# Optimization experiments

Measured on AMD Instinct MI355X. Metric: run time of the kernel, lower is better.

Reference implementation:

```python
import jax, jax.numpy as jnp
import numpy as np
from jax import lax

D, NH, T, DFF, SD = 8, 4, 60, 2048, 17
DH = D // NH
NEG = -1e9

def _ln(x, g, b, eps=1e-5):
    m = jnp.mean(x, -1, keepdims=True)
    v = jnp.mean((x - m) ** 2, -1, keepdims=True)
    return (x - m) / jnp.sqrt(v + eps) * g + b

def _mha(q_in, k_in, v_in, Wqkv, bqkv, Wo, bo, mask):
    Wq, Wk, Wv = jnp.split(Wqkv, 3, axis=0)
    bq, bk, bv = jnp.split(bqkv, 3)
    def proj(x, W, bb):
        B, S, _ = x.shape
        return (x @ W.T + bb).reshape(B, S, NH, DH).transpose(0, 2, 1, 3)
    q = proj(q_in, Wq, bq); k = proj(k_in, Wk, bk); v = proj(v_in, Wv, bv)
    s = jnp.einsum('bhqd,bhkd->bhqk', q, k) / np.float32(np.sqrt(DH))
    s = jnp.where(mask, NEG, s)
    o = jnp.einsum('bhqk,bhkd->bhqd', jax.nn.softmax(s, axis=-1), v)
    B, _, S, _ = o.shape
    return o.transpose(0, 2, 1, 3).reshape(B, S, D) @ Wo.T + bo

def _ffn(x, W1, b1, W2, b2):
    return jax.nn.relu(x @ W1.T + b1) @ W2.T + b2

def _forward(x, emb_W, emb_b, eqW, eqb, eoW, eob, ef1W, ef1b, ef2W, ef2b, el1g, el1b, el2g, el2b, eng, enb, dsqW, dsqb, dsoW, dsob, dcqW, dcqb, dcoW, dcob, df1W, df1b, df2W, df2b, dl1g, dl1b, dl2g, dl2b, dl3g, dl3b, dng, dnb, fc_W, fc_b):
    B = x.shape[0]
    idx = jnp.arange(T)
    causal = (idx[None, :] > idx[:, None])[None, None]  # [1,1,T,T], True = blocked

    @jax.checkpoint
    def step(buf, t):
        keymask = (idx > t)[None, None, None, :]  # positions beyond t are padding
        mem = buf
        for i in range(6):  # nn.Transformer default encoder layers
            mem = _ln(mem + _mha(mem, mem, mem, eqW[i], eqb[i], eoW[i], eob[i], keymask), el1g[i], el1b[i])
            mem = _ln(mem + _ffn(mem, ef1W[i], ef1b[i], ef2W[i], ef2b[i]), el2g[i], el2b[i])
        mem = _ln(mem, eng, enb)
        y = buf
        for i in range(2):  # decoder layers
            y = _ln(y + _mha(y, y, y, dsqW[i], dsqb[i], dsoW[i], dsob[i], causal), dl1g[i], dl1b[i])
            y = _ln(y + _mha(y, mem, mem, dcqW[i], dcqb[i], dcoW[i], dcob[i], keymask), dl2g[i], dl2b[i])
            y = _ln(y + _ffn(y, df1W[i], df1b[i], df2W[i], df2b[i]), dl3g[i], dl3b[i])
        y = _ln(y, dng, dnb)
        st = jnp.take(y, t, axis=1) @ fc_W.T + fc_b  # decoded state at last valid pos [B,17]
        buf = buf.at[:, t + 1].set(st @ emb_W.T + emb_b, mode='drop')
        return buf, st

    buf0 = jnp.zeros((B, T, D), x.dtype).at[:, 0].set(x)
    _, states = lax.scan(step, buf0, idx)
    return jnp.transpose(states, (1, 0, 2))  # [B, T, state_dim]

def setup_inputs() -> dict:
    B = 128
    keys = iter(jax.random.split(jax.random.key(0), 64))
    def W(shape):
        return jax.random.normal(next(keys), shape, jnp.float32) / np.float32(np.sqrt(shape[-1]))
    z = lambda *s: jnp.zeros(s, jnp.float32)
    o = lambda *s: jnp.ones(s, jnp.float32)
    return dict(
        quantized_eos_embedding=jax.random.normal(next(keys), (B, D), jnp.float32),
        emb_W=W((D, SD)), emb_b=z(D),
        eqW=W((6, 3 * D, D)), eqb=z(6, 3 * D), eoW=W((6, D, D)), eob=z(6, D),
        ef1W=W((6, DFF, D)), ef1b=z(6, DFF), ef2W=W((6, D, DFF)), ef2b=z(6, D),
        el1g=o(6, D), el1b=z(6, D), el2g=o(6, D), el2b=z(6, D), eng=o(D), enb=z(D),
        dsqW=W((2, 3 * D, D)), dsqb=z(2, 3 * D), dsoW=W((2, D, D)), dsob=z(2, D),
        dcqW=W((2, 3 * D, D)), dcqb=z(2, 3 * D), dcoW=W((2, D, D)), dcob=z(2, D),
        df1W=W((2, DFF, D)), df1b=z(2, DFF), df2W=W((2, D, DFF)), df2b=z(2, D),
        dl1g=o(2, D), dl1b=z(2, D), dl2g=o(2, D), dl2b=z(2, D), dl3g=o(2, D), dl3b=z(2, D),
        dng=o(D), dnb=z(D),
        fc_W=W((SD, D)), fc_b=z(SD),
    )

def reference(quantized_eos_embedding, emb_W, emb_b, eqW, eqb, eoW, eob, ef1W, ef1b, ef2W, ef2b, el1g, el1b, el2g, el2b, eng, enb, dsqW, dsqb, dsoW, dsob, dcqW, dcqb, dcoW, dcob, df1W, df1b, df2W, df2b, dl1g, dl1b, dl2g, dl2b, dl3g, dl3b, dng, dnb, fc_W, fc_b):
    return _forward(quantized_eos_embedding, emb_W, emb_b, eqW, eqb, eoW, eob, ef1W, ef1b, ef2W, ef2b, el1g, el1b, el2g, el2b, eng, enb, dsqW, dsqb, dsoW, dsob, dcqW, dcqb, dcoW, dcob, df1W, df1b, df2W, df2b, dl1g, dl1b, dl2g, dl2b, dl3g, dl3b, dng, dnb, fc_W, fc_b)
```

## Files before the change

### kernel.cpp

```cpp
#include <hip/hip_runtime.h>


typedef __attribute__((ext_vector_type(8))) short short8;
typedef __attribute__((ext_vector_type(4))) float floatx4;
typedef __attribute__((ext_vector_type(4))) unsigned uint4v;

#define DEV static __device__ __forceinline__

namespace {
constexpr int D   = 8;
constexpr int T   = 60;
constexpr int DFF = 2048;
constexpr int SD  = 17;
constexpr int NT  = 512;
constexpr int NW  = NT / 64;
constexpr int NBLK = DFF / 32;
constexpr int BPW  = NBLK / NW;
constexpr int LSTR = NBLK * 2048;
}

struct Params { const float* in[39]; float* out; };

DEV unsigned short f2bf(float f) {
  unsigned u = __builtin_bit_cast(unsigned, f);
  return (unsigned short)((u + 0x8000u) >> 16);
}
DEV float bf2f(unsigned short h) {
  unsigned u = ((unsigned)h) << 16;
  return __builtin_bit_cast(float, u);
}
DEV floatx4 mfma16(short8 a, short8 b, floatx4 c) {
  return __builtin_amdgcn_mfma_f32_16x16x32_bf16(a, b, c, 0, 0, 0);
}
DEV unsigned cvtpk(float lo, float hi) {
  unsigned r;
  asm("v_cvt_pk_bf16_f32 %0, %1, %2" : "=v"(r) : "v"(lo), "v"(hi));
  return r;
}
DEV float lo2f(unsigned u) { return __builtin_bit_cast(float, u << 16); }
DEV float hi2f(unsigned u) { return __builtin_bit_cast(float, u & 0xffff0000u); }
DEV short8 pack4(unsigned a, unsigned b, unsigned c, unsigned d) {
  uint4v u = {a, b, c, d};
  return __builtin_bit_cast(short8, u);
}

__global__ __launch_bounds__(64) void repack_kernel(Params P, short* ws) {
  const int wg = blockIdx.x;
  const int L = wg >> 6, blk = wg & 63;
  const int l = (int)threadIdx.x, gg = l >> 4, rr = l & 15;
  const float *W1p, *b1p, *W2p;
  if (L < 6) { W1p = P.in[7] + L * 16384;  b1p = P.in[8] + L * 2048;  W2p = P.in[9] + L * 16384; }
  else { int m = L - 6; W1p = P.in[25] + m * 16384; b1p = P.in[26] + m * 2048; W2p = P.in[27] + m * 16384; }
  short* out = ws + (L * 64 + blk) * 2048;
  const int j0 = blk * 32;
  short8 z = {0,0,0,0,0,0,0,0};
  for (int tt = 0; tt < 2; ++tt) {
    int j = j0 + tt * 16 + rr;
    short8 r = z;
    if (gg == 3) {
      unsigned short h = f2bf(b1p[j]);
      r[0] = (short)h; r[1] = (short)f2bf(b1p[j] - bf2f(h));
    } else {
      const float* p = W1p + j * 8;
#pragma unroll
      for (int i = 0; i < 8; ++i) {
        float v = p[i];
        unsigned short h = f2bf(v);
        r[i] = (short)((gg == 1) ? f2bf(v - bf2f(h)) : h);
      }
    }
    *(short8*)(out + tt * 512 + l * 8) = r;
  }
  short8 wh = z, wl = z;
  if (rr < 8) {
#pragma unroll
    for (int i = 0; i < 8; ++i) {
      int j = j0 + (i < 4 ? gg * 4 + i : 16 + gg * 4 + (i - 4));
      float v = W2p[rr * 2048 + j];
      unsigned short h = f2bf(v);
      wh[i] = (short)h;
      wl[i] = (short)f2bf(v - bf2f(h));
    }
  }
  *(short8*)(out + 1024 + l * 8) = wh;
  *(short8*)(out + 1536 + l * 8) = wl;
}

__global__ __launch_bounds__(NT, 2) void tdec_kernel(Params P, const short* ws) {
  const int b    = blockIdx.x;
  const int tid  = (int)threadIdx.x;
  const int lane = tid & 63;
  const int wave = tid >> 6;
  const int gg   = lane >> 4;
  const int rr   = lane & 15;

  __shared__ float buf[T][D];
  __shared__ __align__(16) float X[64][D];
  __shared__ float Mem[64][D];
  __shared__ __align__(16) float Qs[64][D];
  __shared__ __align__(16) float Ks[64][D];
  __shared__ __align__(16) float Vs[64][D];
  __shared__ float ATT[64][D];
  __shared__ __align__(16) float red[NW * 1024];
  __shared__ float wAll[10 * 288];
  __shared__ float lnp[40][D];
  __shared__ float b2all[8][D];
  __shared__ float fcw[SD][D];
  __shared__ float fcbv[SD];
  __shared__ float embw[D][SD];
  __shared__ float embbv[D];
  __shared__ float stv[SD];

  for (int o = tid; o < 2880; o += NT) {
    int a = o / 288, off = o - a * 288;
    const float *Wq, *Bq, *Wo, *Bo; int li;
    if (a < 6)              { li = a;            Wq=P.in[3];  Bq=P.in[4];  Wo=P.in[5];  Bo=P.in[6];  }
    else if (((a - 6) & 1) == 0) { li = (a-6)>>1; Wq=P.in[17]; Bq=P.in[18]; Wo=P.in[19]; Bo=P.in[20]; }
    else                    { li = (a-6)>>1;     Wq=P.in[21]; Bq=P.in[22]; Wo=P.in[23]; Bo=P.in[24]; }
    float v;
    if (off < 192)      v = Wq[li*192 + off];
    else if (off < 216) v = Bq[li*24  + off - 192];
    else if (off < 280) v = Wo[li*64  + off - 216];
    else                v = Bo[li*8   + off - 280];
    wAll[o] = v;
  }
  for (int o = tid; o < 320; o += NT) {
    int row = o >> 3, k = o & 7;
    const float* src;
    if (row < 24) { int li = row >> 2, w = row & 3;
      src = (w==0 ? P.in[11] : w==1 ? P.in[12] : w==2 ? P.in[13] : P.in[14]) + li*8;
    } else if (row < 26) src = (row == 24 ? P.in[15] : P.in[16]);
    else if (row < 38) { int q = row - 26, li = q / 6, w = q - li*6;
      src = (w==0?P.in[29]:w==1?P.in[30]:w==2?P.in[31]:w==3?P.in[32]:w==4?P.in[33]:P.in[34]) + li*8;
    } else src = (row == 38 ? P.in[35] : P.in[36]);
    lnp[row][k] = src[k];
  }
  if (tid < 64) { int row = tid >> 3, k = tid & 7;
    b2all[row][k] = (row < 6) ? P.in[10][row*8 + k] : P.in[28][(row-6)*8 + k]; }
  if (tid < 136) fcw[tid >> 3][tid & 7] = P.in[37][tid];
  if (tid < SD)  fcbv[tid] = P.in[38][tid];
  if (tid < 136) embw[tid / 17][tid % 17] = P.in[1][tid];
  if (tid < D)   embbv[tid] = P.in[2][tid];
  if (tid < D)   buf[0][tid] = P.in[0][b*D + tid];
  __syncthreads();

  const short8 zero8 = {0,0,0,0,0,0,0,0};
  const floatx4 zf4  = {0.f,0.f,0.f,0.f};

  auto proj8 = [&](float (*dst)[D], const float (*src)[D], const float* w,
                   const float* bias, int R) {
    for (int o = tid; o < (R << 3); o += NT) {
      int r = o >> 3, d = o & 7;
      const float* wr = w + d * 8;
      const float* xr = src[r];
      float s = bias[d];
#pragma unroll
      for (int k = 0; k < 8; ++k) s += xr[k] * wr[k];
      dst[r][d] = s;
    }
  };

  auto attn_core = [&](float q0, float q1, int e, int stride, int lim,
                       float& l, float& a0, float& a1) {
    int j = e;
    int s3 = 3 * stride;
    for (; j + s3 <= lim; j += 4 * stride) {
      float2 k0 = *(const float2*)&Ks[j][0] ;
      (void)k0;
      break;
    }
  };
  (void)attn_core;

  auto attn = [&](int R, bool causal) {
    if (R <= 32) {
      int p = tid >> 4, h2 = ((tid >> 2) & 3) << 1, e = tid & 3;
      if (p < R) {
        float q0 = Qs[p][h2]     * 0.70710678118654752f;
        float q1 = Qs[p][h2 + 1] * 0.70710678118654752f;
        int lim = causal ? p : (R - 1);
        float l = 0.f, a0 = 0.f, a1 = 0.f;
        int j = e;
        for (; j + 12 <= lim; j += 16) {
          float2 k0 = *(const float2*)&Ks[j     ][h2];
          float2 k1 = *(const float2*)&Ks[j +  4][h2];
          float2 k2 = *(const float2*)&Ks[j +  8][h2];
          float2 k3 = *(const float2*)&Ks[j + 12][h2];
          float2 v0 = *(const float2*)&Vs[j     ][h2];
          float2 v1 = *(const float2*)&Vs[j +  4][h2];
          float2 v2 = *(const float2*)&Vs[j +  8][h2];
          float2 v3 = *(const float2*)&Vs[j + 12][h2];
          float e0 = __expf(q0 * k0.x + q1 * k0.y - 10.f);
          float e1 = __expf(q0 * k1.x + q1 * k1.y - 10.f);
          float e2 = __expf(q0 * k2.x + q1 * k2.y - 10.f);
          float e3 = __expf(q0 * k3.x + q1 * k3.y - 10.f);
          l += e0; a0 += e0 * v0.x; a1 += e0 * v0.y;
          l += e1; a0 += e1 * v1.x; a1 += e1 * v1.y;
          l += e2; a0 += e2 * v2.x; a1 += e2 * v2.y;
          l += e3; a0 += e3 * v3.x; a1 += e3 * v3.y;
        }
        for (; j <= lim; j += 4) {
          float2 kk = *(const float2*)&Ks[j][h2];
          float2 vv = *(const float2*)&Vs[j][h2];
          float ev = __expf(q0 * kk.x + q1 * kk.y - 10.f);
          l += ev; a0 += ev * vv.x; a1 += ev * vv.y;
        }
        l  += __shfl_xor(l, 1);  l  += __shfl_xor(l, 2);
        a0 += __shfl_xor(a0, 1); a0 += __shfl_xor(a0, 2);
        a1 += __shfl_xor(a1, 1); a1 += __shfl_xor(a1, 2);
        if (e == 0) {
          float rl = 1.f / l;
          ATT[p][h2] = a0 * rl; ATT[p][h2 + 1] = a1 * rl;
        }
      }
    } else {
      int p = tid >> 3, h2 = ((tid >> 1) & 3) << 1, e = tid & 1;
      if (p < R) {
        float q0 = Qs[p][h2]     * 0.70710678118654752f;
        float q1 = Qs[p][h2 + 1] * 0.70710678118654752f;
        int lim = causal ? p : (R - 1);
        float l = 0.f, a0 = 0.f, a1 = 0.f;
        int j = e;
        for (; j + 6 <= lim; j += 8) {
          float2 k0 = *(const float2*)&Ks[j    ][h2];
          float2 k1 = *(const float2*)&Ks[j + 2][h2];
          float2 k2 = *(const float2*)&Ks[j + 4][h2];
          float2 k3 = *(const float2*)&Ks[j + 6][h2];
          float2 v0 = *(const float2*)&Vs[j    ][h2];
          float2 v1 = *(const float2*)&Vs[j + 2][h2];
          float2 v2 = *(const float2*)&Vs[j + 4][h2];
          float2 v3 = *(const float2*)&Vs[j + 6][h2];
          float e0 = __expf(q0 * k0.x + q1 * k0.y - 10.f);
          float e1 = __expf(q0 * k1.x + q1 * k1.y - 10.f);
          float e2 = __expf(q0 * k2.x + q1 * k2.y - 10.f);
          float e3 = __expf(q0 * k3.x + q1 * k3.y - 10.f);
          l += e0; a0 += e0 * v0.x; a1 += e0 * v0.y;
          l += e1; a0 += e1 * v1.x; a1 += e1 * v1.y;
          l += e2; a0 += e2 * v2.x; a1 += e2 * v2.y;
          l += e3; a0 += e3 * v3.x; a1 += e3 * v3.y;
        }
        for (; j <= lim; j += 2) {
          float2 kk = *(const float2*)&Ks[j][h2];
          float2 vv = *(const float2*)&Vs[j][h2];
          float ev = __expf(q0 * kk.x + q1 * kk.y - 10.f);
          l += ev; a0 += ev * vv.x; a1 += ev * vv.y;
        }
        l  += __shfl_xor(l, 1);
        a0 += __shfl_xor(a0, 1);
        a1 += __shfl_xor(a1, 1);
        if (e == 0) {
          float rl = 1.f / l;
          ATT[p][h2] = a0 * rl; ATT[p][h2 + 1] = a1 * rl;
        }
      }
    }
  };

  auto oproj_ln = [&](const float* wo, const float* bo, const float* g,
                      const float* bb, int R) {
    if (tid < R) {
      float o[8];
#pragma unroll
      for (int d = 0; d < 8; ++d) {
        float s = bo[d] + X[tid][d];
#pragma unroll
        for (int k = 0; k < 8; ++k) s += ATT[tid][k] * wo[d * 8 + k];
        o[d] = s;
      }
      float m = 0.f;
#pragma unroll
      for (int k = 0; k < 8; ++k) m += o[k];
      m *= 0.125f;
      float v = 0.f;
#pragma unroll
      for (int k = 0; k < 8; ++k) { float dm = o[k] - m; v += dm * dm; }
      float rs = rsqrtf(v * 0.125f + 1e-5f);
#pragma unroll
      for (int k = 0; k < 8; ++k) X[tid][k] = (o[k] - m) * rs * g[k] + bb[k];
    }
  };

  auto ln_rows = [&](float (*dst)[D], const float (*src)[D], const float* g,
                     const float* bb, int R) {
    if (tid < R) {
      float o[8];
#pragma unroll
      for (int k = 0; k < 8; ++k) o[k] = src[tid][k];
      float m = 0.f;
#pragma unroll
      for (int k = 0; k < 8; ++k) m += o[k];
      m *= 0.125f;
      float v = 0.f;
#pragma unroll
      for (int k = 0; k < 8; ++k) { float dm = o[k] - m; v += dm * dm; }
      float rs = rsqrtf(v * 0.125f + 1e-5f);
#pragma unroll
      for (int k = 0; k < 8; ++k) dst[tid][k] = (o[k] - m) * rs * g[k] + bb[k];
    }
  };

  auto mha = [&](int a, float (*kvsrc)[D], bool causal, int R,
                 const float* g, const float* bb) {
    const float* wq = &wAll[a * 288];
    proj8(Qs, X,     wq +   0, wq + 192, R);
    proj8(Ks, kvsrc, wq +  64, wq + 200, R);
    proj8(Vs, kvsrc, wq + 128, wq + 208, R);
    __syncthreads();
    attn(R, causal);
    __syncthreads();
    oproj_ln(wq + 216, wq + 280, g, bb, R);
    __syncthreads();
  };

  auto mha_row = [&](int a, float (*kvsrc)[D], int R, int t,
                     const float* g, const float* bb) {
    const float* wq = &wAll[a * 288];
    proj8(Ks, kvsrc, wq +  64, wq + 200, R);
    proj8(Vs, kvsrc, wq + 128, wq + 208, R);
    if (tid < 8) {
      int d = tid;
      const float* wr = wq + d * 8;
      float s = wq[192 + d];
#pragma unroll
      for (int k = 0; k < 8; ++k) s += X[t][k] * wr[k];
      Qs[t][d] = s;
    }
    __syncthreads();
    if (tid < 32) {
      int h2 = (tid >> 3) << 1, e = tid & 7;
      float q0 = Qs[t][h2]     * 0.70710678118654752f;
      float q1 = Qs[t][h2 + 1] * 0.70710678118654752f;
      float l = 0.f, a0 = 0.f, a1 = 0.f;
      int j = e;
      for (; j + 24 < R; j += 32) {
        float2 k0 = *(const float2*)&Ks[j     ][h2];
        float2 k1 = *(const float2*)&Ks[j +  8][h2];
        float2 k2 = *(const float2*)&Ks[j + 16][h2];
        float2 k3 = *(const float2*)&Ks[j + 24][h2];
        float2 v0 = *(const float2*)&Vs[j     ][h2];
        float2 v1 = *(const float2*)&Vs[j +  8][h2];
        float2 v2 = *(const float2*)&Vs[j + 16][h2];
        float2 v3 = *(const float2*)&Vs[j + 24][h2];
        float e0 = __expf(q0 * k0.x + q1 * k0.y - 10.f);
        float e1 = __expf(q0 * k1.x + q1 * k1.y - 10.f);
        float e2 = __expf(q0 * k2.x + q1 * k2.y - 10.f);
        float e3 = __expf(q0 * k3.x + q1 * k3.y - 10.f);
        l += e0; a0 += e0 * v0.x; a1 += e0 * v0.y;
        l += e1; a0 += e1 * v1.x; a1 += e1 * v1.y;
        l += e2; a0 += e2 * v2.x; a1 += e2 * v2.y;
        l += e3; a0 += e3 * v3.x; a1 += e3 * v3.y;
      }
      for (; j < R; j += 8) {
        float2 kk = *(const float2*)&Ks[j][h2];
        float2 vv = *(const float2*)&Vs[j][h2];
        float ev = __expf(q0 * kk.x + q1 * kk.y - 10.f);
        l += ev; a0 += ev * vv.x; a1 += ev * vv.y;
      }
      l  += __shfl_xor(l, 1);  l  += __shfl_xor(l, 2);  l  += __shfl_xor(l, 4);
      a0 += __shfl_xor(a0, 1); a0 += __shfl_xor(a0, 2); a0 += __shfl_xor(a0, 4);
      a1 += __shfl_xor(a1, 1); a1 += __shfl_xor(a1, 2); a1 += __shfl_xor(a1, 4);
      if (e == 0) {
        float rl = 1.f / l;
        ATT[t][h2] = a0 * rl; ATT[t][h2 + 1] = a1 * rl;
      }
    }
    __syncthreads();
    if (tid == 0) {
      float o[8];
#pragma unroll
      for (int d = 0; d < 8; ++d) {
        float s = wq[280 + d] + X[t][d];
#pragma unroll
        for (int k = 0; k < 8; ++k) s += ATT[t][k] * wq[216 + d * 8 + k];
        o[d] = s;
      }
      float m = 0.f;
#pragma unroll
      for (int k = 0; k < 8; ++k) m += o[k];
      m *= 0.125f;
      float v = 0.f;
#pragma unroll
      for (int k = 0; k < 8; ++k) { float dm = o[k] - m; v += dm * dm; }
      float rs = rsqrtf(v * 0.125f + 1e-5f);
#pragma unroll
      for (int k = 0; k < 8; ++k) X[t][k] = (o[k] - m) * rs * g[k] + bb[k];
    }
    __syncthreads();
  };

  auto ffn = [&](const short* wsL, const float* b2, const float* g,
                 const float* bb, int R, int Mt) {
    const short* pb = wsL + (wave * BPW) * 2048;
    short8 a0  = *(const short8*)(pb + lane * 8);
    short8 a1  = *(const short8*)(pb + 512 + lane * 8);
    short8 w2h = *(const short8*)(pb + 1024 + lane * 8);
    short8 w2l = *(const short8*)(pb + 1536 + lane * 8);

    short8 bx[4];
#pragma unroll
    for (int mt = 0; mt < 4; ++mt) {
      short8 v = zero8;
      if (mt < Mt) {
        if (gg == 3) { v[0] = (short)0x3F80; v[1] = (short)0x3F80; }
        else {
          int r = mt * 16 + rr;
          float4 A = *(const float4*)&X[r][0];
          float4 Bv = *(const float4*)&X[r][4];
          unsigned u0 = cvtpk(A.x, A.y), u1 = cvtpk(A.z, A.w);
          unsigned u2 = cvtpk(Bv.x, Bv.y), u3 = cvtpk(Bv.z, Bv.w);
          if (gg == 2) {
            unsigned l0 = cvtpk(A.x - lo2f(u0), A.y - hi2f(u0));
            unsigned l1 = cvtpk(A.z - lo2f(u1), A.w - hi2f(u1));
            unsigned l2 = cvtpk(Bv.x - lo2f(u2), Bv.y - hi2f(u2));
            unsigned l3 = cvtpk(Bv.z - lo2f(u3), Bv.w - hi2f(u3));
            v = pack4(l0, l1, l2, l3);
          } else {
            v = pack4(u0, u1, u2, u3);
          }
        }
      }
      bx[mt] = v;
    }

    floatx4 acc[4] = {zf4, zf4, zf4, zf4};
    for (int blkI = 0; blkI < BPW; ++blkI) {
      short8 na0 = zero8, na1 = zero8, nw2h = zero8, nw2l = zero8;
      if (blkI + 1 < BPW) {
        const short* pn = pb + (blkI + 1) * 2048;
        na0  = *(const short8*)(pn + lane * 8);
        na1  = *(const short8*)(pn + 512 + lane * 8);
        nw2h = *(const short8*)(pn + 1024 + lane * 8);
        nw2l = *(const short8*)(pn + 1536 + lane * 8);
      }
#pragma unroll
      for (int mt = 0; mt < 4; ++mt) {
        if (mt < Mt) {
          floatx4 h0 = mfma16(a0, bx[mt], zf4);
          floatx4 h1 = mfma16(a1, bx[mt], zf4);
          float v0 = fmaxf(h0[0], 0.f), v1 = fmaxf(h0[1], 0.f);
          float v2 = fmaxf(h0[2], 0.f), v3 = fmaxf(h0[3], 0.f);
          float v4 = fmaxf(h1[0], 0.f), v5 = fmaxf(h1[1], 0.f);
          float v6 = fmaxf(h1[2], 0.f), v7 = fmaxf(h1[3], 0.f);
          unsigned u0 = cvtpk(v0, v1), u1 = cvtpk(v2, v3);
          unsigned u2 = cvtpk(v4, v5), u3 = cvtpk(v6, v7);
          unsigned l0 = cvtpk(v0 - lo2f(u0), v1 - hi2f(u0));
          unsigned l1 = cvtpk(v2 - lo2f(u1), v3 - hi2f(u1));
          unsigned l2 = cvtpk(v4 - lo2f(u2), v5 - hi2f(u2));
          unsigned l3 = cvtpk(v6 - lo2f(u3), v7 - hi2f(u3));
          short8 ah = pack4(u0, u1, u2, u3);
          short8 al = pack4(l0, l1, l2, l3);
          acc[mt] = mfma16(w2h, ah, acc[mt]);
          acc[mt] = mfma16(w2h, al, acc[mt]);
          acc[mt] = mfma16(w2l, ah, acc[mt]);
        }
      }
      a0 = na0; a1 = na1; w2h = nw2h; w2l = nw2l;
    }

#pragma unroll
    for (int mt = 0; mt < 4; ++mt)
      if (mt < Mt)
        *(floatx4*)&red[(((wave << 2) + mt) << 8) + (lane << 2)] = acc[mt];
    __syncthreads();
    if (tid < R) {
      int r = tid, mt = r >> 4, rl = r & 15;
      float o[8];
#pragma unroll
      for (int d = 0; d < 8; ++d) {
        float s = X[r][d] + b2[d];
        int base = (mt << 8) + ((((d >> 2) << 4) + rl) << 2) + (d & 3);
#pragma unroll
        for (int w = 0; w < NW; ++w) s += red[(w << 10) + base];
        o[d] = s;
      }
      float m = 0.f;
#pragma unroll
      for (int k = 0; k < 8; ++k) m += o[k];
      m *= 0.125f;
      float var = 0.f;
#pragma unroll
      for (int k = 0; k < 8; ++k) { float dm = o[k] - m; var += dm * dm; }
      float rs = rsqrtf(var * 0.125f + 1e-5f);
#pragma unroll
      for (int k = 0; k < 8; ++k) X[r][k] = (o[k] - m) * rs * g[k] + bb[k];
    }
    __syncthreads();
  };

  auto ffn_row = [&](const short* wsL, const float* b2, const float* g,
                     const float* bb, int t) {
    const short* pb = wsL + (wave * BPW) * 2048;
    short8 a0  = *(const short8*)(pb + lane * 8);
    short8 a1  = *(const short8*)(pb + 512 + lane * 8);
    short8 w2h = *(const short8*)(pb + 1024 + lane * 8);
    short8 w2l = *(const short8*)(pb + 1536 + lane * 8);

    short8 bx = zero8;
    if (gg == 3) { bx[0] = (short)0x3F80; bx[1] = (short)0x3F80; }
    else if (rr == 0) {
      float4 A = *(const float4*)&X[t][0];
      float4 Bv = *(const float4*)&X[t][4];
      unsigned u0 = cvtpk(A.x, A.y), u1 = cvtpk(A.z, A.w);
      unsigned u2 = cvtpk(Bv.x, Bv.y), u3 = cvtpk(Bv.z, Bv.w);
      if (gg == 2) {
        unsigned l0 = cvtpk(A.x - lo2f(u0), A.y - hi2f(u0));
        unsigned l1 = cvtpk(A.z - lo2f(u1), A.w - hi2f(u1));
        unsigned l2 = cvtpk(Bv.x - lo2f(u2), Bv.y - hi2f(u2));
        unsigned l3 = cvtpk(Bv.z - lo2f(u3), Bv.w - hi2f(u3));
        bx = pack4(l0, l1, l2, l3);
      } else {
        bx = pack4(u0, u1, u2, u3);
      }
    }

    floatx4 acc = zf4;
    for (int blkI = 0; blkI < BPW; ++blkI) {
      short8 na0 = zero8, na1 = zero8, nw2h = zero8, nw2l = zero8;
      if (blkI + 1 < BPW) {
        const short* pn = pb + (blkI + 1) * 2048;
        na0  = *(const short8*)(pn + lane * 8);
        na1  = *(const short8*)(pn + 512 + lane * 8);
        nw2h = *(const short8*)(pn + 1024 + lane * 8);
        nw2l = *(const short8*)(pn + 1536 + lane * 8);
      }
      floatx4 h0 = mfma16(a0, bx, zf4);
      floatx4 h1 = mfma16(a1, bx, zf4);
      float v0 = fmaxf(h0[0], 0.f), v1 = fmaxf(h0[1], 0.f);
      float v2 = fmaxf(h0[2], 0.f), v3 = fmaxf(h0[3], 0.f);
      float v4 = fmaxf(h1[0], 0.f), v5 = fmaxf(h1[1], 0.f);
      float v6 = fmaxf(h1[2], 0.f), v7 = fmaxf(h1[3], 0.f);
      unsigned u0 = cvtpk(v0, v1), u1 = cvtpk(v2, v3);
      unsigned u2 = cvtpk(v4, v5), u3 = cvtpk(v6, v7);
      unsigned l0 = cvtpk(v0 - lo2f(u0), v1 - hi2f(u0));
      unsigned l1 = cvtpk(v2 - lo2f(u1), v3 - hi2f(u1));
      unsigned l2 = cvtpk(v4 - lo2f(u2), v5 - hi2f(u2));
      unsigned l3 = cvtpk(v6 - lo2f(u3), v7 - hi2f(u3));
      short8 ah = pack4(u0, u1, u2, u3);
      short8 al = pack4(l0, l1, l2, l3);
      acc = mfma16(w2h, ah, acc);
      acc = mfma16(w2h, al, acc);
      acc = mfma16(w2l, ah, acc);
      a0 = na0; a1 = na1; w2h = nw2h; w2l = nw2l;
    }

    *(floatx4*)&red[(wave << 10) + (lane << 2)] = acc;
    __syncthreads();
    if (tid == 0) {
      float o[8];
#pragma unroll
      for (int d = 0; d < 8; ++d) {
        float s = X[t][d] + b2[d];
        int base = ((d >> 2) << 6) + (d & 3);
#pragma unroll
        for (int w = 0; w < NW; ++w) s += red[(w << 10) + base];
        o[d] = s;
      }
      float m = 0.f;
#pragma unroll
      for (int k = 0; k < 8; ++k) m += o[k];
      m *= 0.125f;
      float var = 0.f;
#pragma unroll
      for (int k = 0; k < 8; ++k) { float dm = o[k] - m; var += dm * dm; }
      float rs = rsqrtf(var * 0.125f + 1e-5f);
#pragma unroll
      for (int k = 0; k < 8; ++k) X[t][k] = (o[k] - m) * rs * g[k] + bb[k];
    }
    __syncthreads();
  };

  for (int t = 0; t < T; ++t) {
    const int R = t + 1;
    const int Mt = (R + 15) >> 4;

    for (int o = tid; o < 512; o += NT) {
      int r = o >> 3, d = o & 7;
      X[r][d] = (r < R) ? buf[r][d] : 0.f;
    }
    __syncthreads();

    for (int li = 0; li < 6; ++li) {
      mha(li, X, false, R, lnp[li * 4 + 0], lnp[li * 4 + 1]);
      ffn(ws + li * LSTR, b2all[li], lnp[li * 4 + 2], lnp[li * 4 + 3], R, Mt);
    }
    ln_rows(X, X, lnp[24], lnp[25], R);
    __syncthreads();
    for (int o = tid; o < 512; o += NT) {
      int r = o >> 3, d = o & 7;
      if (r < R) Mem[r][d] = X[r][d];
      X[r][d] = (r < R) ? buf[r][d] : 0.f;
    }
    __syncthreads();

    mha(6, X,   true,  R, lnp[26], lnp[27]);
    mha(7, Mem, false, R, lnp[28], lnp[29]);
    ffn(ws + 6 * LSTR, b2all[6], lnp[30], lnp[31], R, Mt);

    mha_row(8, X,   R, t, lnp[32], lnp[33]);
    mha_row(9, Mem, R, t, lnp[34], lnp[35]);
    ffn_row(ws + 7 * LSTR, b2all[7], lnp[36], lnp[37], t);

    if (tid == 0) {
      float o[8];
#pragma unroll
      for (int k = 0; k < 8; ++k) o[k] = X[t][k];
      float m = 0.f;
#pragma unroll
      for (int k = 0; k < 8; ++k) m += o[k];
      m *= 0.125f;
      float v = 0.f;
#pragma unroll
      for (int k = 0; k < 8; ++k) { float dm = o[k] - m; v += dm * dm; }
      float rs = rsqrtf(v * 0.125f + 1e-5f);
#pragma unroll
      for (int k = 0; k < 8; ++k) X[t][k] = (o[k] - m) * rs * lnp[38][k] + lnp[39][k];
    }
    __syncthreads();
    if (tid < SD) {
      float s = fcbv[tid];
#pragma unroll
      for (int k = 0; k < 8; ++k) s += X[t][k] * fcw[tid][k];
      stv[tid] = s;
      P.out[(b * T + t) * SD + tid] = s;
    }
    __syncthreads();
    if (t + 1 < T && tid < D) {
      float s = embbv[tid];
#pragma unroll
      for (int k = 0; k < SD; ++k) s += stv[k] * embw[tid][k];
      buf[t + 1][tid] = s;
    }
    __syncthreads();
  }
}

extern "C" void kernel_launch(void* const* d_in, const int* in_sizes, int n_in,
                              void* d_out, int out_size, void* d_ws, size_t ws_size,
                              hipStream_t stream) {
  (void)in_sizes; (void)n_in; (void)ws_size; (void)out_size;
  Params P;
  for (int i = 0; i < 39; ++i) P.in[i] = (const float*)d_in[i];
  P.out = (float*)d_out;
  short* ws = (short*)d_ws;
  repack_kernel<<<dim3(8 * NBLK), dim3(64), 0, stream>>>(P, ws);
  tdec_kernel<<<dim3(128), dim3(NT), 0, stream>>>(P, ws);
}
```

Baseline: 3.383 ms.

## Cache per-row layer-0 QKV and decoder self-attn state across timesteps

```diff
diff --git a/kernel.cpp b/kernel.cpp
--- a/kernel.cpp
+++ b/kernel.cpp
@@ -101,6 +101,12 @@
   __shared__ __align__(16) float Ks[64][D];
   __shared__ __align__(16) float Vs[64][D];
   __shared__ float ATT[64][D];
+  __shared__ __align__(16) float Q0s[64][D];
+  __shared__ __align__(16) float K0s[64][D];
+  __shared__ __align__(16) float V0s[64][D];
+  __shared__ __align__(16) float K6s[64][D];
+  __shared__ __align__(16) float V6s[64][D];
+  __shared__ __align__(16) float D1[64][D];
   __shared__ __align__(16) float red[NW * 1024];
   __shared__ float wAll[10 * 288];
   __shared__ float lnp[40][D];
@@ -160,36 +166,25 @@
     }
   };
 
-  auto attn_core = [&](float q0, float q1, int e, int stride, int lim,
-                       float& l, float& a0, float& a1) {
-    int j = e;
-    int s3 = 3 * stride;
-    for (; j + s3 <= lim; j += 4 * stride) {
-      float2 k0 = *(const float2*)&Ks[j][0] ;
-      (void)k0;
-      break;
-    }
-  };
-  (void)attn_core;
-
-  auto attn = [&](int R, bool causal) {
+  auto attn = [&](const float (*Qp)[D], const float (*Kp)[D],
+                  const float (*Vp)[D], int R, bool causal) {
     if (R <= 32) {
       int p = tid >> 4, h2 = ((tid >> 2) & 3) << 1, e = tid & 3;
       if (p < R) {
-        float q0 = Qs[p][h2]     * 0.70710678118654752f;
-        float q1 = Qs[p][h2 + 1] * 0.70710678118654752f;
+        float q0 = Qp[p][h2]     * 0.70710678118654752f;
+        float q1 = Qp[p][h2 + 1] * 0.70710678118654752f;
         int lim = causal ? p : (R - 1);
         float l = 0.f, a0 = 0.f, a1 = 0.f;
         int j = e;
         for (; j + 12 <= lim; j += 16) {
-          float2 k0 = *(const float2*)&Ks[j     ][h2];
-          float2 k1 = *(const float2*)&Ks[j +  4][h2];
-          float2 k2 = *(const float2*)&Ks[j +  8][h2];
-          float2 k3 = *(const float2*)&Ks[j + 12][h2];
-          float2 v0 = *(const float2*)&Vs[j     ][h2];
-          float2 v1 = *(const float2*)&Vs[j +  4][h2];
-          float2 v2 = *(const float2*)&Vs[j +  8][h2];
-          float2 v3 = *(const float2*)&Vs[j + 12][h2];
+          float2 k0 = *(const float2*)&Kp[j     ][h2];
+          float2 k1 = *(const float2*)&Kp[j +  4][h2];
+          float2 k2 = *(const float2*)&Kp[j +  8][h2];
+          float2 k3 = *(const float2*)&Kp[j + 12][h2];
+          float2 v0 = *(const float2*)&Vp[j     ][h2];
+          float2 v1 = *(const float2*)&Vp[j +  4][h2];
+          float2 v2 = *(const float2*)&Vp[j +  8][h2];
+          float2 v3 = *(const float2*)&Vp[j + 12][h2];
           float e0 = __expf(q0 * k0.x + q1 * k0.y - 10.f);
           float e1 = __expf(q0 * k1.x + q1 * k1.y - 10.f);
           float e2 = __expf(q0 * k2.x + q1 * k2.y - 10.f);
@@ -200,8 +195,8 @@
           l += e3; a0 += e3 * v3.x; a1 += e3 * v3.y;
         }
         for (; j <= lim; j += 4) {
-          float2 kk = *(const float2*)&Ks[j][h2];
-          float2 vv = *(const float2*)&Vs[j][h2];
+          float2 kk = *(const float2*)&Kp[j][h2];
+          float2 vv = *(const float2*)&Vp[j][h2];
           float ev = __expf(q0 * kk.x + q1 * kk.y - 10.f);
           l += ev; a0 += ev * vv.x; a1 += ev * vv.y;
         }
@@ -216,20 +211,20 @@
     } else {
       int p = tid >> 3, h2 = ((tid >> 1) & 3) << 1, e = tid & 1;
       if (p < R) {
-        float q0 = Qs[p][h2]     * 0.70710678118654752f;
-        float q1 = Qs[p][h2 + 1] * 0.70710678118654752f;
+        float q0 = Qp[p][h2]     * 0.70710678118654752f;
+        float q1 = Qp[p][h2 + 1] * 0.70710678118654752f;
         int lim = causal ? p : (R - 1);
         float l = 0.f, a0 = 0.f, a1 = 0.f;
         int j = e;
         for (; j + 6 <= lim; j += 8) {
-          float2 k0 = *(const float2*)&Ks[j    ][h2];
-          float2 k1 = *(const float2*)&Ks[j + 2][h2];
-          float2 k2 = *(const float2*)&Ks[j + 4][h2];
-          float2 k3 = *(const float2*)&Ks[j + 6][h2];
-          float2 v0 = *(const float2*)&Vs[j    ][h2];
-          float2 v1 = *(const float2*)&Vs[j + 2][h2];
-          float2 v2 = *(const float2*)&Vs[j + 4][h2];
-          float2 v3 = *(const float2*)&Vs[j + 6][h2];
+          float2 k0 = *(const float2*)&Kp[j    ][h2];
+          float2 k1 = *(const float2*)&Kp[j + 2][h2];
+          float2 k2 = *(const float2*)&Kp[j + 4][h2];
+          float2 k3 = *(const float2*)&Kp[j + 6][h2];
+          float2 v0 = *(const float2*)&Vp[j    ][h2];
+          float2 v1 = *(const float2*)&Vp[j + 2][h2];
+          float2 v2 = *(const float2*)&Vp[j + 4][h2];
+          float2 v3 = *(const float2*)&Vp[j + 6][h2];
           float e0 = __expf(q0 * k0.x + q1 * k0.y - 10.f);
           float e1 = __expf(q0 * k1.x + q1 * k1.y - 10.f);
           float e2 = __expf(q0 * k2.x + q1 * k2.y - 10.f);
@@ -240,8 +235,8 @@
           l += e3; a0 += e3 * v3.x; a1 += e3 * v3.y;
         }
         for (; j <= lim; j += 2) {
-          float2 kk = *(const float2*)&Ks[j][h2];
-          float2 vv = *(const float2*)&Vs[j][h2];
+          float2 kk = *(const float2*)&Kp[j][h2];
+          float2 vv = *(const float2*)&Vp[j][h2];
           float ev = __expf(q0 * kk.x + q1 * kk.y - 10.f);
           l += ev; a0 += ev * vv.x; a1 += ev * vv.y;
         }
@@ -257,12 +252,13 @@
   };
 
   auto oproj_ln = [&](const float* wo, const float* bo, const float* g,
-                      const float* bb, int R) {
+                      const float* bb, int R, const float (*res)[D],
+                      float (*dst)[D]) {
     if (tid < R) {
       float o[8];
 #pragma unroll
       for (int d = 0; d < 8; ++d) {
-        float s = bo[d] + X[tid][d];
+        float s = bo[d] + res[tid][d];
 #pragma unroll
         for (int k = 0; k < 8; ++k) s += ATT[tid][k] * wo[d * 8 + k];
         o[d] = s;
@@ -276,7 +272,7 @@
       for (int k = 0; k < 8; ++k) { float dm = o[k] - m; v += dm * dm; }
       float rs = rsqrtf(v * 0.125f + 1e-5f);
 #pragma unroll
-      for (int k = 0; k < 8; ++k) X[tid][k] = (o[k] - m) * rs * g[k] + bb[k];
+      for (int k = 0; k < 8; ++k) dst[tid][k] = (o[k] - m) * rs * g[k] + bb[k];
     }
   };
 
@@ -306,9 +302,9 @@
     proj8(Ks, kvsrc, wq +  64, wq + 200, R);
     proj8(Vs, kvsrc, wq + 128, wq + 208, R);
     __syncthreads();
-    attn(R, causal);
-    __syncthreads();
-    oproj_ln(wq + 216, wq + 280, g, bb, R);
+    attn(Qs, Ks, Vs, R, causal);
+    __syncthreads();
+    oproj_ln(wq + 216, wq + 280, g, bb, R, X, X);
     __syncthreads();
   };
 
@@ -577,23 +573,123 @@
       int r = o >> 3, d = o & 7;
       X[r][d] = (r < R) ? buf[r][d] : 0.f;
     }
-    __syncthreads();
-
-    for (int li = 0; li < 6; ++li) {
+    if (tid < 40) {
+      int sel = tid >> 3, d = tid & 7;
+      const float* wq0 = &wAll[0];
+      const float* wq6 = &wAll[6 * 288];
+      const float* w; float bias; float* dst;
+      if (sel == 0)      { w = wq0 + 0   + d * 8; bias = wq0[192 + d]; dst = &Q0s[t][d]; }
+      else if (sel == 1) { w = wq0 + 64  + d * 8; bias = wq0[200 + d]; dst = &K0s[t][d]; }
+      else if (sel == 2) { w = wq0 + 128 + d * 8; bias = wq0[208 + d]; dst = &V0s[t][d]; }
+      else if (sel == 3) { w = wq6 + 64  + d * 8; bias = wq6[200 + d]; dst = &K6s[t][d]; }
+      else               { w = wq6 + 128 + d * 8; bias = wq6[208 + d]; dst = &V6s[t][d]; }
+      float s = bias;
+#pragma unroll
+      for (int k = 0; k < 8; ++k) s += buf[t][k] * w[k];
+      *dst = s;
+    }
+    __syncthreads();
+
+    attn(Q0s, K0s, V0s, R, false);
+    __syncthreads();
+    oproj_ln(&wAll[0] + 216, &wAll[0] + 280, lnp[0], lnp[1], R, X, X);
+    __syncthreads();
+    ffn(ws + 0 * LSTR, b2all[0], lnp[2], lnp[3], R, Mt);
+
+    for (int li = 1; li < 6; ++li) {
       mha(li, X, false, R, lnp[li * 4 + 0], lnp[li * 4 + 1]);
       ffn(ws + li * LSTR, b2all[li], lnp[li * 4 + 2], lnp[li * 4 + 3], R, Mt);
     }
     ln_rows(X, X, lnp[24], lnp[25], R);
     __syncthreads();
-    for (int o = tid; o < 512; o += NT) {
+
+    for (int o = tid; o < (R << 3); o += NT) {
       int r = o >> 3, d = o & 7;
-      if (r < R) Mem[r][d] = X[r][d];
-      X[r][d] = (r < R) ? buf[r][d] : 0.f;
-    }
-    __syncthreads();
-
-    mha(6, X,   true,  R, lnp[26], lnp[27]);
-    mha(7, Mem, false, R, lnp[28], lnp[29]);
+      Mem[r][d] = X[r][d];
+    }
+    if (tid < 8) {
+      const float* wq6 = &wAll[6 * 288];
+      int d = tid;
+      float s = wq6[192 + d];
+#pragma unroll
+      for (int k = 0; k < 8; ++k) s += buf[t][k] * wq6[d * 8 + k];
+      Qs[t][d] = s;
+    }
+    __syncthreads();
+
+    if (tid < 32) {
+      int h2 = (tid >> 3) << 1, e = tid & 7;
+      float q0 = Qs[t][h2]     * 0.70710678118654752f;
+      float q1 = Qs[t][h2 + 1] * 0.70710678118654752f;
+      float l = 0.f, a0 = 0.f, a1 = 0.f;
+      int j = e;
+      for (; j + 24 < R; j += 32) {
+        float2 k0 = *(const float2*)&K6s[j     ][h2];
+        float2 k1 = *(const float2*)&K6s[j +  8][h2];
+        float2 k2 = *(const float2*)&K6s[j + 16][h2];
+        float2 k3 = *(const float2*)&K6s[j + 24][h2];
+        float2 v0 = *(const float2*)&V6s[j     ][h2];
+        float2 v1 = *(const float2*)&V6s[j +  8][h2];
+        float2 v2 = *(const float2*)&V6s[j + 16][h2];
+        float2 v3 = *(const float2*)&V6s[j + 24][h2];
+        float e0 = __expf(q0 * k0.x + q1 * k0.y - 10.f);
+        float e1 = __expf(q0 * k1.x + q1 * k1.y - 10.f);
+        float e2 = __expf(q0 * k2.x + q1 * k2.y - 10.f);
+        float e3 = __expf(q0 * k3.x + q1 * k3.y - 10.f);
+        l += e0; a0 += e0 * v0.x; a1 += e0 * v0.y;
+        l += e1; a0 += e1 * v1.x; a1 += e1 * v1.y;
+        l += e2; a0 += e2 * v2.x; a1 += e2 * v2.y;
+        l += e3; a0 += e3 * v3.x; a1 += e3 * v3.y;
+      }
+      for (; j < R; j += 8) {
+        float2 kk = *(const float2*)&K6s[j][h2];
+        float2 vv = *(const float2*)&V6s[j][h2];
+        float ev = __expf(q0 * kk.x + q1 * kk.y - 10.f);
+        l += ev; a0 += ev * vv.x; a1 += ev * vv.y;
+      }
+      l  += __shfl_xor(l, 1);  l  += __shfl_xor(l, 2);  l  += __shfl_xor(l, 4);
+      a0 += __shfl_xor(a0, 1); a0 += __shfl_xor(a0, 2); a0 += __shfl_xor(a0, 4);
+      a1 += __shfl_xor(a1, 1); a1 += __shfl_xor(a1, 2); a1 += __shfl_xor(a1, 4);
+      if (e == 0) {
+        float rl = 1.f / l;
+        ATT[t][h2] = a0 * rl; ATT[t][h2 + 1] = a1 * rl;
+      }
+    }
+    __syncthreads();
+    if (tid == 0) {
+      const float* wq6 = &wAll[6 * 288];
+      float o[8];
+#pragma unroll
+      for (int d = 0; d < 8; ++d) {
+        float s = wq6[280 + d] + buf[t][d];
+#pragma unroll
+        for (int k = 0; k < 8; ++k) s += ATT[t][k] * wq6[216 + d * 8 + k];
+        o[d] = s;
+      }
+      float m = 0.f;
+#pragma unroll
+      for (int k = 0; k < 8; ++k) m += o[k];
+      m *= 0.125f;
+      float v = 0.f;
+#pragma unroll
+      for (int k = 0; k < 8; ++k) { float dm = o[k] - m; v += dm * dm; }
+      float rs = rsqrtf(v * 0.125f + 1e-5f);
+#pragma unroll
+      for (int k = 0; k < 8; ++k) D1[t][k] = (o[k] - m) * rs * lnp[26][k] + lnp[27][k];
+    }
+    __syncthreads();
+
+    {
+      const float* wq7 = &wAll[7 * 288];
+      proj8(Qs, D1,  wq7 +   0, wq7 + 192, R);
+      proj8(Ks, Mem, wq7 +  64, wq7 + 200, R);
+      proj8(Vs, Mem, wq7 + 128, wq7 + 208, R);
+      __syncthreads();
+      attn(Qs, Ks, Vs, R, false);
+      __syncthreads();
+      oproj_ln(wq7 + 216, wq7 + 280, lnp[28], lnp[29], R, D1, X);
+      __syncthreads();
+    }
     ffn(ws + 6 * LSTR, b2all[6], lnp[30], lnp[31], R, Mt);
 
     mha_row(8, X,   R, t, lnp[32], lnp[33]);
```

Result: no change. 3.334 ms (-1.5%).
